# Optimization experiments

Hardware: AMD Instinct MI355X
Metric: run time of the kernel (lower is better)

## Reference

```python
import jax, jax.numpy as jnp
import numpy as np

MARGIN = 1.0
EPS = 1e-05
B = 8192
D = 128
NUM_CLASSES = 256


def setup_inputs() -> dict:
    key = jax.random.key(0)
    k1, k2 = jax.random.split(key)
    feature = jax.random.normal(k1, (B, D), dtype=jnp.float32)
    label = jax.random.randint(k2, (B,), 0, NUM_CLASSES, dtype=jnp.int32)
    return {"feature": feature, "label": label}


def reference(feature, label):
    # Pairwise Euclidean distance matrix: ||x_i||^2 + ||x_j||^2 - 2 x_i.x_j + eps, then sqrt
    sq = jnp.sum(feature * feature, axis=1, keepdims=True)  # [B, 1]
    dist = jnp.sqrt(jnp.maximum(sq + sq.T - 2.0 * (feature @ feature.T) + EPS, 0.0))  # [B, B]

    same = label[:, None] == label[None, :]  # [B, B] bool, includes self on diagonal
    inf = jnp.array(jnp.inf, dtype=dist.dtype)

    # Original sorts each row and takes same[1]: the SECOND smallest same-label distance
    # (the smallest is the anchor itself, distance sqrt(eps)).
    d_same = jnp.where(same, dist, inf)
    two_smallest = -jax.lax.top_k(-d_same, 2)[0]  # [B, 2], ascending smallest two
    pos = two_smallest[:, 1]  # nearest positive excluding self

    # diff.min(): hardest (closest) negative per row
    neg = jnp.min(jnp.where(same, inf, dist), axis=1)

    hinge = jnp.maximum(MARGIN + pos - neg, 0.0)
    return jnp.mean(hinge)
```

## Files before the change

kernel.cpp:

```cpp
#include <hip/hip_runtime.h>
#include <math.h>


#define BN 8192
#define MARGIN_F 1.0f
#define EPS_F 1e-5f

typedef __attribute__((ext_vector_type(8))) short short8;
typedef __attribute__((ext_vector_type(4))) float floatx4;

__device__ __forceinline__ unsigned short bf16_rne(float x, float& r) {
    unsigned u = __float_as_uint(x);
    u += 0x7FFF + ((u >> 16) & 1);
    unsigned short h = (unsigned short)(u >> 16);
    r = __uint_as_float(((unsigned)h) << 16);
    return h;
}

__global__ __launch_bounds__(256) void prep_kernel(const float* __restrict__ f,
                                                   const int* __restrict__ lbl,
                                                   short8* __restrict__ fbT,
                                                   float2* __restrict__ lsq,
                                                   float* __restrict__ g_acc,
                                                   unsigned* __restrict__ counter) {
    int gid = blockIdx.x * 256 + threadIdx.x;
    if (gid == 0) { *g_acc = 0.f; *counter = 0u; }
    int row = gid >> 3, part = gid & 7;
    const float4* f4 = (const float4*)f + (size_t)row * 32 + part * 4;
    float s = 0.f;
#pragma unroll
    for (int cc = 0; cc < 2; ++cc) {
        float4 v0 = f4[cc * 2], v1 = f4[cc * 2 + 1];
        float r0, r1, r2, r3, r4, r5, r6, r7;
        short8 o;
        o[0] = (short)bf16_rne(v0.x, r0);
        o[1] = (short)bf16_rne(v0.y, r1);
        o[2] = (short)bf16_rne(v0.z, r2);
        o[3] = (short)bf16_rne(v0.w, r3);
        o[4] = (short)bf16_rne(v1.x, r4);
        o[5] = (short)bf16_rne(v1.y, r5);
        o[6] = (short)bf16_rne(v1.z, r6);
        o[7] = (short)bf16_rne(v1.w, r7);
        fbT[(size_t)(part * 2 + cc) * BN + row] = o;
        s += r0 * r0 + r1 * r1 + r2 * r2 + r3 * r3 +
             r4 * r4 + r5 * r5 + r6 * r6 + r7 * r7;
    }
    s += __shfl_xor(s, 1, 8);
    s += __shfl_xor(s, 2, 8);
    s += __shfl_xor(s, 4, 8);
    if (part == 0) {
        float2 p;
        p.x = s;
        p.y = __int_as_float(lbl[row]);
        lsq[row] = p;
    }
}

__device__ __forceinline__ void stage_tile(const short8* __restrict__ fbT,
                                           short8* tile, int j0, int wv, int lane) {
#pragma unroll
    for (int it = 0; it < 2; ++it) {
        int s = wv * 128 + it * 64;
        int kc = (s >> 5) + (lane >> 5);
        int col = lane & 31;
        const short8* g = fbT + ((size_t)kc * BN + j0 + col);
        __builtin_amdgcn_global_load_lds(
            (const __attribute__((address_space(1))) void*)g,
            (__attribute__((address_space(3))) void*)(tile + s),
            16, 0, 0);
    }
}

__global__ __launch_bounds__(256, 2) void work_kernel(const short8* __restrict__ fbT,
                                                      const int* __restrict__ lbl,
                                                      const float2* __restrict__ lsq,
                                                      float* __restrict__ part,
                                                      float* __restrict__ pos_d2) {
    const int t = threadIdx.x;
    const int lane = t & 63;
    const int wv = t >> 6;
    const int q = lane >> 4, c = lane & 15;
    const int bid = blockIdx.x;

    if (bid >= 512) {
        __shared__ int midx[256];
        __shared__ int cnt;
        const int cls = bid - 512;
        if (t == 0) cnt = 0;
        __syncthreads();
        const int4* lbl4 = (const int4*)lbl;
        for (int r4 = t; r4 < BN / 4; r4 += 256) {
            int4 L = lbl4[r4];
            if (L.x == cls) { int p = atomicAdd(&cnt, 1); if (p < 256) midx[p] = r4 * 4; }
            if (L.y == cls) { int p = atomicAdd(&cnt, 1); if (p < 256) midx[p] = r4 * 4 + 1; }
            if (L.z == cls) { int p = atomicAdd(&cnt, 1); if (p < 256) midx[p] = r4 * 4 + 2; }
            if (L.w == cls) { int p = atomicAdd(&cnt, 1); if (p < 256) midx[p] = r4 * 4 + 3; }
        }
        __syncthreads();
        int n = cnt < 256 ? cnt : 256;
        if (n == 0) return;
        if (t < 256 && t >= n) midx[t] = midx[0];
        __syncthreads();

        const int ng = (n + 15) >> 4;
        for (int ig = wv; ig < ng; ig += 4) {
            short8 a[4];
            int arow = midx[ig * 16 + c];
#pragma unroll
            for (int ks = 0; ks < 4; ++ks)
                a[ks] = fbT[(size_t)(ks * 4 + q) * BN + arow];
            float s1[4], s2[4];
#pragma unroll
            for (int rg = 0; rg < 4; ++rg) { s1[rg] = INFINITY; s2[rg] = INFINITY; }

            for (int s = 0; s < ng; ++s) {
                int jslot = s * 16 + c;
                int jrow = midx[jslot];
                short8 b[4];
#pragma unroll
                for (int ks = 0; ks < 4; ++ks)
                    b[ks] = fbT[(size_t)(ks * 4 + q) * BN + jrow];
                float sj = lsq[jrow].x;
                bool valid = (jslot < n);

                floatx4 acc = (floatx4)0.f;
#pragma unroll
                for (int ks = 0; ks < 4; ++ks)
                    acc = __builtin_amdgcn_mfma_f32_16x16x32_bf16(a[ks], b[ks], acc, 0, 0, 0);
#pragma unroll
                for (int rg = 0; rg < 4; ++rg) {
                    float v = fmaf(-2.0f, acc[rg], sj);
                    float vs = valid ? v : INFINITY;
                    s2[rg] = fminf(s2[rg], fmaxf(s1[rg], vs));
                    s1[rg] = fminf(s1[rg], vs);
                }
            }
#pragma unroll
            for (int m = 1; m < 16; m <<= 1) {
#pragma unroll
                for (int rg = 0; rg < 4; ++rg) {
                    float o1 = __shfl_xor(s1[rg], m, 16);
                    float o2 = __shfl_xor(s2[rg], m, 16);
                    float lo = fminf(s1[rg], o1);
                    float hi = fminf(fmaxf(s1[rg], o1), fminf(s2[rg], o2));
                    s1[rg] = lo; s2[rg] = hi;
                }
            }
            if (c == 0) {
#pragma unroll
                for (int rg = 0; rg < 4; ++rg) {
                    int islot = ig * 16 + q * 4 + rg;
                    if (islot < n) {
                        int row = midx[islot];
                        pos_d2[row] = lsq[row].x + s2[rg];
                    }
                }
            }
        }
        return;
    }

    __shared__ short8 Bt[2][512];
    __shared__ float2 lsq_sh[512];

    const int i0 = (bid & 31) * 256 + wv * 64;
    const int g = bid >> 5;
    const int jb = g * 512;

    stage_tile(fbT, Bt[0], jb, wv, lane);

    lsq_sh[t] = lsq[jb + t];
    lsq_sh[t + 256] = lsq[jb + t + 256];

    short8 a[4][4];
#pragma unroll
    for (int mf = 0; mf < 4; ++mf) {
        int row = i0 + mf * 16 + c;
#pragma unroll
        for (int ks = 0; ks < 4; ++ks)
            a[mf][ks] = fbT[(size_t)(ks * 4 + q) * BN + row];
    }
    int li[4][4];
#pragma unroll
    for (int mf = 0; mf < 4; ++mf)
#pragma unroll
        for (int rg = 0; rg < 4; ++rg)
            li[mf][rg] = __float_as_int(lsq[i0 + mf * 16 + q * 4 + rg].y);

    float n1[4][4];
#pragma unroll
    for (int mf = 0; mf < 4; ++mf)
#pragma unroll
        for (int rg = 0; rg < 4; ++rg) n1[mf][rg] = INFINITY;

    __syncthreads();

    for (int jt = 0; jt < 16; ++jt) {
        const short8* cur = Bt[jt & 1];
        const int j0 = jb + jt * 32;
        if (jt < 15) stage_tile(fbT, Bt[1 - (jt & 1)], j0 + 32, wv, lane);

        int ljv[2]; float sjv[2];
#pragma unroll
        for (int nf = 0; nf < 2; ++nf) {
            float2 p = lsq_sh[jt * 32 + nf * 16 + c];
            sjv[nf] = p.x;
            ljv[nf] = __float_as_int(p.y);
        }

        floatx4 acc[4][2];
#pragma unroll
        for (int mf = 0; mf < 4; ++mf)
#pragma unroll
            for (int nf = 0; nf < 2; ++nf) acc[mf][nf] = (floatx4)0.f;

#pragma unroll
        for (int ks = 0; ks < 4; ++ks) {
            short8 b[2];
#pragma unroll
            for (int nf = 0; nf < 2; ++nf)
                b[nf] = cur[(ks * 4 + q) * 32 + nf * 16 + c];
#pragma unroll
            for (int mf = 0; mf < 4; ++mf)
#pragma unroll
                for (int nf = 0; nf < 2; ++nf)
                    acc[mf][nf] = __builtin_amdgcn_mfma_f32_16x16x32_bf16(
                        a[mf][ks], b[nf], acc[mf][nf], 0, 0, 0);
        }

#pragma unroll
        for (int nf = 0; nf < 2; ++nf) {
#pragma unroll
            for (int mf = 0; mf < 4; ++mf)
#pragma unroll
                for (int rg = 0; rg < 4; ++rg) {
                    float v = fmaf(-2.0f, acc[mf][nf][rg], sjv[nf]);
                    float vd = (li[mf][rg] == ljv[nf]) ? INFINITY : v;
                    n1[mf][rg] = fminf(n1[mf][rg], vd);
                }
        }
        __syncthreads();
    }

#pragma unroll
    for (int m = 1; m < 16; m <<= 1) {
#pragma unroll
        for (int mf = 0; mf < 4; ++mf)
#pragma unroll
            for (int rg = 0; rg < 4; ++rg)
                n1[mf][rg] = fminf(n1[mf][rg], __shfl_xor(n1[mf][rg], m, 16));
    }
    if (c == 0) {
#pragma unroll
        for (int mf = 0; mf < 4; ++mf)
#pragma unroll
            for (int rg = 0; rg < 4; ++rg)
                part[g * BN + i0 + mf * 16 + q * 4 + rg] = n1[mf][rg];
    }
}

__global__ __launch_bounds__(128) void merge_kernel(const float* __restrict__ part,
                                                    const float2* __restrict__ lsq,
                                                    const float* __restrict__ pos_d2,
                                                    float* __restrict__ g_acc,
                                                    unsigned* __restrict__ counter,
                                                    float* __restrict__ out) {
    int r = blockIdx.x * 128 + threadIdx.x;
    float n = INFINITY;
#pragma unroll
    for (int k = 0; k < 16; ++k) n = fminf(n, part[k * BN + r]);
    float si = lsq[r].x;
    float pos = sqrtf(fmaxf(pos_d2[r] + EPS_F, 0.f));
    float neg = sqrtf(fmaxf(si + n + EPS_F, 0.f));
    float h = fmaxf(MARGIN_F + pos - neg, 0.f);
    __shared__ float red[2];
#pragma unroll
    for (int m = 32; m >= 1; m >>= 1) h += __shfl_down(h, m, 64);
    if ((threadIdx.x & 63) == 0) red[threadIdx.x >> 6] = h;
    __syncthreads();
    if (threadIdx.x == 0) {
        atomicAdd(g_acc, red[0] + red[1]);
        __threadfence();
        unsigned old = atomicAdd(counter, 1u);
        if (old == 63u) {
            float tot = atomicAdd(g_acc, 0.0f);
            out[0] = tot / (float)BN;
        }
    }
}

extern "C" void kernel_launch(void* const* d_in, const int* in_sizes, int n_in,
                              void* d_out, int out_size, void* d_ws, size_t ws_size,
                              hipStream_t stream) {
    const float* f = (const float*)d_in[0];
    const int* lbl = (const int*)d_in[1];
    char* ws = (char*)d_ws;
    float2* lsq = (float2*)ws;
    short8* fbT = (short8*)(ws + 65536);
    float* part = (float*)(ws + 65536 + 2097152);
    float* pos_d2 = (float*)(ws + 65536 + 2097152 + 524288);
    float* g_acc = (float*)(ws + 65536 + 2097152 + 524288 + 32768);
    unsigned* counter = (unsigned*)(g_acc + 1);
    float* out = (float*)d_out;

    prep_kernel<<<256, 256, 0, stream>>>(f, lbl, fbT, lsq, g_acc, counter);
    work_kernel<<<768, 256, 0, stream>>>(fbT, lbl, lsq, part, pos_d2);
    merge_kernel<<<64, 128, 0, stream>>>(part, lsq, pos_d2, g_acc, counter, out);
}
```

Baseline: 83.51 us.

## Fold per-class positive search into the dense negative-distance sweep

Removes the 256 extra per-class blocks that gathered same-label rows and recomputed their distances. The dense all-pairs tile loop now also tracks the two smallest same-label distances per row, and the merge kernel combines these per-tile partials across the 16 column groups. This drops the irregular gather work and the label scan. In exchange it adds more VALU work and registers in the hot loop and three times the partial-result traffic.

```diff
diff --git a/kernel.cpp b/kernel.cpp
--- a/kernel.cpp
+++ b/kernel.cpp
@@ -72,94 +72,16 @@
 }
 
 __global__ __launch_bounds__(256, 2) void work_kernel(const short8* __restrict__ fbT,
-                                                      const int* __restrict__ lbl,
                                                       const float2* __restrict__ lsq,
-                                                      float* __restrict__ part,
-                                                      float* __restrict__ pos_d2) {
+                                                      float* __restrict__ part_n1,
+                                                      float* __restrict__ part_s1,
+                                                      float* __restrict__ part_s2) {
     const int t = threadIdx.x;
     const int lane = t & 63;
     const int wv = t >> 6;
     const int q = lane >> 4, c = lane & 15;
     const int bid = blockIdx.x;
 
-    if (bid >= 512) {
-        __shared__ int midx[256];
-        __shared__ int cnt;
-        const int cls = bid - 512;
-        if (t == 0) cnt = 0;
-        __syncthreads();
-        const int4* lbl4 = (const int4*)lbl;
-        for (int r4 = t; r4 < BN / 4; r4 += 256) {
-            int4 L = lbl4[r4];
-            if (L.x == cls) { int p = atomicAdd(&cnt, 1); if (p < 256) midx[p] = r4 * 4; }
-            if (L.y == cls) { int p = atomicAdd(&cnt, 1); if (p < 256) midx[p] = r4 * 4 + 1; }
-            if (L.z == cls) { int p = atomicAdd(&cnt, 1); if (p < 256) midx[p] = r4 * 4 + 2; }
-            if (L.w == cls) { int p = atomicAdd(&cnt, 1); if (p < 256) midx[p] = r4 * 4 + 3; }
-        }
-        __syncthreads();
-        int n = cnt < 256 ? cnt : 256;
-        if (n == 0) return;
-        if (t < 256 && t >= n) midx[t] = midx[0];
-        __syncthreads();
-
-        const int ng = (n + 15) >> 4;
-        for (int ig = wv; ig < ng; ig += 4) {
-            short8 a[4];
-            int arow = midx[ig * 16 + c];
-#pragma unroll
-            for (int ks = 0; ks < 4; ++ks)
-                a[ks] = fbT[(size_t)(ks * 4 + q) * BN + arow];
-            float s1[4], s2[4];
-#pragma unroll
-            for (int rg = 0; rg < 4; ++rg) { s1[rg] = INFINITY; s2[rg] = INFINITY; }
-
-            for (int s = 0; s < ng; ++s) {
-                int jslot = s * 16 + c;
-                int jrow = midx[jslot];
-                short8 b[4];
-#pragma unroll
-                for (int ks = 0; ks < 4; ++ks)
-                    b[ks] = fbT[(size_t)(ks * 4 + q) * BN + jrow];
-                float sj = lsq[jrow].x;
-                bool valid = (jslot < n);
-
-                floatx4 acc = (floatx4)0.f;
-#pragma unroll
-                for (int ks = 0; ks < 4; ++ks)
-                    acc = __builtin_amdgcn_mfma_f32_16x16x32_bf16(a[ks], b[ks], acc, 0, 0, 0);
-#pragma unroll
-                for (int rg = 0; rg < 4; ++rg) {
-                    float v = fmaf(-2.0f, acc[rg], sj);
-                    float vs = valid ? v : INFINITY;
-                    s2[rg] = fminf(s2[rg], fmaxf(s1[rg], vs));
-                    s1[rg] = fminf(s1[rg], vs);
-                }
-            }
-#pragma unroll
-            for (int m = 1; m < 16; m <<= 1) {
-#pragma unroll
-                for (int rg = 0; rg < 4; ++rg) {
-                    float o1 = __shfl_xor(s1[rg], m, 16);
-                    float o2 = __shfl_xor(s2[rg], m, 16);
-                    float lo = fminf(s1[rg], o1);
-                    float hi = fminf(fmaxf(s1[rg], o1), fminf(s2[rg], o2));
-                    s1[rg] = lo; s2[rg] = hi;
-                }
-            }
-            if (c == 0) {
-#pragma unroll
-                for (int rg = 0; rg < 4; ++rg) {
-                    int islot = ig * 16 + q * 4 + rg;
-                    if (islot < n) {
-                        int row = midx[islot];
-                        pos_d2[row] = lsq[row].x + s2[rg];
-                    }
-                }
-            }
-        }
-        return;
-    }
-
     __shared__ short8 Bt[2][512];
     __shared__ float2 lsq_sh[512];
 
@@ -187,11 +109,15 @@
         for (int rg = 0; rg < 4; ++rg)
             li[mf][rg] = __float_as_int(lsq[i0 + mf * 16 + q * 4 + rg].y);
 
-    float n1[4][4];
+    float n1[4][4], s1[4][4], s2[4][4];
 #pragma unroll
     for (int mf = 0; mf < 4; ++mf)
 #pragma unroll
-        for (int rg = 0; rg < 4; ++rg) n1[mf][rg] = INFINITY;
+        for (int rg = 0; rg < 4; ++rg) {
+            n1[mf][rg] = INFINITY;
+            s1[mf][rg] = INFINITY;
+            s2[mf][rg] = INFINITY;
+        }
 
     __syncthreads();
 
@@ -235,8 +161,12 @@
 #pragma unroll
                 for (int rg = 0; rg < 4; ++rg) {
                     float v = fmaf(-2.0f, acc[mf][nf][rg], sjv[nf]);
-                    float vd = (li[mf][rg] == ljv[nf]) ? INFINITY : v;
+                    bool same = (li[mf][rg] == ljv[nf]);
+                    float vd = same ? INFINITY : v;
+                    float vs = same ? v : INFINITY;
                     n1[mf][rg] = fminf(n1[mf][rg], vd);
+                    s2[mf][rg] = fminf(s2[mf][rg], fmaxf(s1[mf][rg], vs));
+                    s1[mf][rg] = fminf(s1[mf][rg], vs);
                 }
         }
         __syncthreads();
@@ -247,30 +177,47 @@
 #pragma unroll
         for (int mf = 0; mf < 4; ++mf)
 #pragma unroll
-            for (int rg = 0; rg < 4; ++rg)
+            for (int rg = 0; rg < 4; ++rg) {
                 n1[mf][rg] = fminf(n1[mf][rg], __shfl_xor(n1[mf][rg], m, 16));
+                float o1 = __shfl_xor(s1[mf][rg], m, 16);
+                float o2 = __shfl_xor(s2[mf][rg], m, 16);
+                float hi = fminf(fmaxf(s1[mf][rg], o1), fminf(s2[mf][rg], o2));
+                s1[mf][rg] = fminf(s1[mf][rg], o1);
+                s2[mf][rg] = hi;
+            }
     }
     if (c == 0) {
 #pragma unroll
         for (int mf = 0; mf < 4; ++mf)
 #pragma unroll
-            for (int rg = 0; rg < 4; ++rg)
-                part[g * BN + i0 + mf * 16 + q * 4 + rg] = n1[mf][rg];
-    }
-}
-
-__global__ __launch_bounds__(128) void merge_kernel(const float* __restrict__ part,
+            for (int rg = 0; rg < 4; ++rg) {
+                int idx = g * BN + i0 + mf * 16 + q * 4 + rg;
+                part_n1[idx] = n1[mf][rg];
+                part_s1[idx] = s1[mf][rg];
+                part_s2[idx] = s2[mf][rg];
+            }
+    }
+}
+
+__global__ __launch_bounds__(128) void merge_kernel(const float* __restrict__ part_n1,
+                                                    const float* __restrict__ part_s1,
+                                                    const float* __restrict__ part_s2,
                                                     const float2* __restrict__ lsq,
-                                                    const float* __restrict__ pos_d2,
                                                     float* __restrict__ g_acc,
                                                     unsigned* __restrict__ counter,
                                                     float* __restrict__ out) {
     int r = blockIdx.x * 128 + threadIdx.x;
-    float n = INFINITY;
-#pragma unroll
-    for (int k = 0; k < 16; ++k) n = fminf(n, part[k * BN + r]);
+    float n = INFINITY, s1 = INFINITY, s2 = INFINITY;
+#pragma unroll
+    for (int k = 0; k < 16; ++k) {
+        n = fminf(n, part_n1[k * BN + r]);
+        float a1 = part_s1[k * BN + r];
+        float a2 = part_s2[k * BN + r];
+        s2 = fminf(fmaxf(s1, a1), fminf(s2, a2));
+        s1 = fminf(s1, a1);
+    }
     float si = lsq[r].x;
-    float pos = sqrtf(fmaxf(pos_d2[r] + EPS_F, 0.f));
+    float pos = sqrtf(fmaxf(si + s2 + EPS_F, 0.f));
     float neg = sqrtf(fmaxf(si + n + EPS_F, 0.f));
     float h = fmaxf(MARGIN_F + pos - neg, 0.f);
     __shared__ float red[2];
@@ -297,13 +244,14 @@
     char* ws = (char*)d_ws;
     float2* lsq = (float2*)ws;
     short8* fbT = (short8*)(ws + 65536);
-    float* part = (float*)(ws + 65536 + 2097152);
-    float* pos_d2 = (float*)(ws + 65536 + 2097152 + 524288);
-    float* g_acc = (float*)(ws + 65536 + 2097152 + 524288 + 32768);
+    float* part_n1 = (float*)(ws + 65536 + 2097152);
+    float* part_s1 = (float*)(ws + 65536 + 2097152 + 524288);
+    float* part_s2 = (float*)(ws + 65536 + 2097152 + 1048576);
+    float* g_acc = (float*)(ws + 65536 + 2097152 + 1572864);
     unsigned* counter = (unsigned*)(g_acc + 1);
     float* out = (float*)d_out;
 
     prep_kernel<<<256, 256, 0, stream>>>(f, lbl, fbT, lsq, g_acc, counter);
-    work_kernel<<<768, 256, 0, stream>>>(fbT, lbl, lsq, part, pos_d2);
-    merge_kernel<<<64, 128, 0, stream>>>(part, lsq, pos_d2, g_acc, counter, out);
-}
+    work_kernel<<<512, 256, 0, stream>>>(fbT, lsq, part_n1, part_s1, part_s2);
+    merge_kernel<<<64, 128, 0, stream>>>(part_n1, part_s1, part_s2, lsq, g_acc, counter, out);
+}
```

Measured after the change: 94.69 us. +13.4%, slower.
